# Performance work log

Measured on AMD Instinct MI355X. Metric: run time of the kernel, lower is better.

The kernel has to match this reference:

```python
import jax, jax.numpy as jnp
import numpy as np

N = 20000          # nodes
F = 64             # num_features
H = 128            # hidden_channels
K = 6              # kNN neighbors (includes self, matching torch_cluster.knn(x, x, k))
E = 120000         # unused edge_index length


def knn_indices(x, k):
    # squared euclidean pairwise distances: [N, N]
    sq = jnp.sum(x * x, axis=-1)
    dist2 = sq[:, None] + sq[None, :] - 2.0 * (x @ x.T)
    # k smallest distances per row (self included, dist ~0)
    _, idx = jax.lax.top_k(-dist2, k)   # [N, K]
    return idx


def setup_inputs() -> dict:
    key = jax.random.key(0)
    ks = jax.random.split(key, 6)
    x = jax.random.normal(ks[0], (N, F), dtype=jnp.float32)
    edge_index = jax.random.randint(ks[1], (2, E), 0, N, dtype=jnp.int64)
    W1 = jax.random.normal(ks[2], (2 * F, H), dtype=jnp.float32) * 0.05
    b1 = jnp.zeros((H,), dtype=jnp.float32)
    W2 = jax.random.normal(ks[3], (H, H), dtype=jnp.float32) * 0.05
    b2 = jnp.zeros((H,), dtype=jnp.float32)
    return {"x": x, "edge_index": edge_index, "W1": W1, "b1": b1, "W2": W2, "b2": b2}


def reference(x, edge_index, W1, b1, W2, b2):
    # DynamicEdgeConv: recompute kNN graph each forward (edge_index arg unused, as in source)
    idx = knn_indices(x, K)                       # [N, K] neighbor indices j for each center i
    xi = jnp.broadcast_to(x[:, None, :], (N, K, F))  # center features
    xj = x[idx]                                   # neighbor features  [N, K, F]
    msg = jnp.concatenate([xi, xj - xi], axis=-1)    # [N, K, 2F]
    h = jax.nn.relu(jnp.einsum('nkf,fh->nkh', msg, W1) + b1)
    h = jnp.einsum('nkh,hg->nkg', h, W2) + b2     # [N, K, H]
    return jnp.max(h, axis=1)                     # max aggregation -> [N, H]
```

## Files before the change

kernel.cpp:

```cpp
#include <hip/hip_runtime.h>


#define N_NODES 20000
#define FDIM 64
#define KNN 6
#define HID 128
#define N_PAD 20480
#define NTILES 625
#define PREP_TILES 628
#define NBLK 157
#define NCHUNK 3
#define TPC 209
#define RPB 256
#define TILE_J 64
#define MAX_CHUNKS 10

typedef __attribute__((ext_vector_type(8))) short short8;
typedef __attribute__((ext_vector_type(16))) float f32x16;

#define MFMAB(A, B, C) __builtin_amdgcn_mfma_f32_32x32x16_bf16((A), (B), (C), 0, 0, 0)
#define ROFF(r) (((r) & 3) + 8 * ((r) >> 2))

#define INSERT_CAND(bd, bj, dv, jv) do {                                      \
  if ((dv) < bd[5]) {                                                         \
    const bool c0 = (dv) < bd[0], c1 = (dv) < bd[1], c2 = (dv) < bd[2];       \
    const bool c3 = (dv) < bd[3], c4 = (dv) < bd[4];                          \
    bd[5] = c4 ? bd[4] : (dv);              bj[5] = c4 ? bj[4] : (jv);        \
    bd[4] = c4 ? (c3 ? bd[3] : (dv)) : bd[4]; bj[4] = c4 ? (c3 ? bj[3] : (jv)) : bj[4]; \
    bd[3] = c3 ? (c2 ? bd[2] : (dv)) : bd[3]; bj[3] = c3 ? (c2 ? bj[2] : (jv)) : bj[3]; \
    bd[2] = c2 ? (c1 ? bd[1] : (dv)) : bd[2]; bj[2] = c2 ? (c1 ? bj[1] : (jv)) : bj[2]; \
    bd[1] = c1 ? (c0 ? bd[0] : (dv)) : bd[1]; bj[1] = c1 ? (c0 ? bj[0] : (jv)) : bj[1]; \
    bd[0] = c0 ? (dv) : bd[0];              bj[0] = c0 ? (jv) : bj[0];        \
  }                                                                           \
} while (0)

#define LEXLT(dv, jv, ds, js) (((dv) < (ds)) || ((dv) == (ds) && (jv) < (js)))
#define INSERT_TIE(bd, bj, dv, jv) do {                                       \
  if (LEXLT((dv), (jv), bd[5], bj[5])) {                                      \
    const bool c0 = LEXLT((dv), (jv), bd[0], bj[0]);                          \
    const bool c1 = LEXLT((dv), (jv), bd[1], bj[1]);                          \
    const bool c2 = LEXLT((dv), (jv), bd[2], bj[2]);                          \
    const bool c3 = LEXLT((dv), (jv), bd[3], bj[3]);                          \
    const bool c4 = LEXLT((dv), (jv), bd[4], bj[4]);                          \
    bd[5] = c4 ? bd[4] : (dv);              bj[5] = c4 ? bj[4] : (jv);        \
    bd[4] = c4 ? (c3 ? bd[3] : (dv)) : bd[4]; bj[4] = c4 ? (c3 ? bj[3] : (jv)) : bj[4]; \
    bd[3] = c3 ? (c2 ? bd[2] : (dv)) : bd[3]; bj[3] = c3 ? (c2 ? bj[2] : (jv)) : bj[3]; \
    bd[2] = c2 ? (c1 ? bd[1] : (dv)) : bd[2]; bj[2] = c2 ? (c1 ? bj[1] : (jv)) : bj[2]; \
    bd[1] = c1 ? (c0 ? bd[0] : (dv)) : bd[1]; bj[1] = c1 ? (c0 ? bj[0] : (jv)) : bj[1]; \
    bd[0] = c0 ? (dv) : bd[0];              bj[0] = c0 ? (jv) : bj[0];        \
  }                                                                           \
} while (0)

__device__ __forceinline__ f32x16 zero16() {
  f32x16 v;
#pragma unroll
  for (int i = 0; i < 16; ++i) v[i] = 0.f;
  return v;
}

__device__ __forceinline__ unsigned short bf16_rne(float x) {
  unsigned u = __float_as_uint(x);
  u += 0x7fffu + ((u >> 16) & 1u);
  return (unsigned short)(u >> 16);
}
__device__ __forceinline__ float bf16_tof(unsigned short h) {
  return __uint_as_float(((unsigned)h) << 16);
}

__device__ __forceinline__ void gload_lds16(const void* g, void* l) {
  __builtin_amdgcn_global_load_lds(
      (const __attribute__((address_space(1))) void*)g,
      (__attribute__((address_space(3))) void*)l, 16, 0, 0);
}

__global__ void prep_kernel(const float* __restrict__ x, short* __restrict__ xa,
                            short* __restrict__ xb, short* __restrict__ xc,
                            float* __restrict__ sq) {
  const int n = blockIdx.x * blockDim.x + threadIdx.x;
  if (n >= PREP_TILES * 32) return;
  const int tile = n >> 5, row = n & 31;
  unsigned short a[FDIM], b[FDIM], c[FDIM];
  float s = 0.f;
  if (n < N_NODES) {
    const float4* r4 = (const float4*)(x + (size_t)n * FDIM);
#pragma unroll
    for (int q = 0; q < 16; ++q) {
      const float4 v = r4[q];
      const float vv[4] = {v.x, v.y, v.z, v.w};
#pragma unroll
      for (int e = 0; e < 4; ++e) {
        const float xv = vv[e];
        s = fmaf(xv, xv, s);
        const unsigned short ua = bf16_rne(xv);
        const float r1 = xv - bf16_tof(ua);
        const unsigned short ub = bf16_rne(r1);
        const float r2 = r1 - bf16_tof(ub);
        a[q * 4 + e] = ua; b[q * 4 + e] = ub; c[q * 4 + e] = bf16_rne(r2);
      }
    }
  } else {
#pragma unroll
    for (int f = 0; f < FDIM; ++f) { a[f] = 0; b[f] = 0; c[f] = 0; }
    s = __builtin_inff();
  }
  sq[n] = s;
#pragma unroll
  for (int ks = 0; ks < 4; ++ks) {
#pragma unroll
    for (int hh = 0; hh < 2; ++hh) {
      short8 va, vb, vc;
#pragma unroll
      for (int j = 0; j < 8; ++j) {
        const int f = ks * 16 + hh * 8 + j;
        va[j] = (short)a[f]; vb[j] = (short)b[f]; vc[j] = (short)c[f];
      }
      const size_t off = (size_t)tile * 2048 + ks * 512 + (size_t)((hh << 5) | row) * 8;
      *(short8*)(xa + off) = va;
      *(short8*)(xb + off) = vb;
      *(short8*)(xc + off) = vc;
    }
  }
}

__device__ __forceinline__ void load_frag(const short* __restrict__ xa,
                                          const short* __restrict__ xb,
                                          const short* __restrict__ xc, int t,
                                          int lane, short8 (&Fa)[4],
                                          short8 (&Fb)[4], short8 (&Fc)[4]) {
  const size_t tb = (size_t)t * 2048 + (size_t)lane * 8;
#pragma unroll
  for (int ks = 0; ks < 4; ++ks) {
    Fa[ks] = *(const short8*)(xa + tb + ks * 512);
    Fb[ks] = *(const short8*)(xb + tb + ks * 512);
    Fc[ks] = *(const short8*)(xc + tb + ks * 512);
  }
}

__device__ __forceinline__ void do_select(const f32x16& acc,
                                          const float* __restrict__ sq, int t,
                                          int h, float (&bd)[KNN],
                                          int (&bj)[KNN]) {
  const int sbase = t * 32 + 4 * h;
  float4 S4[4];
#pragma unroll
  for (int g = 0; g < 4; ++g) S4[g] = *(const float4*)(sq + sbase + 8 * g);
  const float sqa[16] = {S4[0].x, S4[0].y, S4[0].z, S4[0].w,
                         S4[1].x, S4[1].y, S4[1].z, S4[1].w,
                         S4[2].x, S4[2].y, S4[2].z, S4[2].w,
                         S4[3].x, S4[3].y, S4[3].z, S4[3].w};
  float key[16];
#pragma unroll
  for (int r = 0; r < 16; ++r) key[r] = fmaf(-2.f, acc[r], sqa[r]);
  float m8[8];
#pragma unroll
  for (int r = 0; r < 8; ++r) m8[r] = fminf(key[r], key[r + 8]);
  float m4[4];
#pragma unroll
  for (int r = 0; r < 4; ++r) m4[r] = fminf(m8[r], m8[r + 4]);
  const float m2a = fminf(m4[0], m4[2]), m2b = fminf(m4[1], m4[3]);
  const float m = fminf(m2a, m2b);
  if (__any(m < bd[5])) {
    const int jbase = t * 32 + 4 * h;
#pragma unroll
    for (int r = 0; r < 16; ++r) { INSERT_CAND(bd, bj, key[r], jbase + ROFF(r)); }
  }
}

__device__ __forceinline__ void xmerge(float (&bd)[KNN], int (&bj)[KNN]) {
  float od[KNN];
  int oj[KNN];
#pragma unroll
  for (int k = 0; k < KNN; ++k) {
    od[k] = __shfl_xor(bd[k], 32);
    oj[k] = __shfl_xor(bj[k], 32);
  }
#pragma unroll
  for (int k = 0; k < KNN; ++k) INSERT_TIE(bd, bj, od[k], oj[k]);
}

__global__ __launch_bounds__(256, 2) void knn_bf16_kernel(
    const short* __restrict__ xa, const short* __restrict__ xb,
    const short* __restrict__ xc, const float* __restrict__ sq,
    float* __restrict__ cand_d, unsigned short* __restrict__ cand_js,
    int* __restrict__ knn_idx, int nchunks) {
  __shared__ __align__(16) short sa[2][2048];
  __shared__ __align__(16) short sb[2][2048];
  __shared__ __align__(16) short sc[2][2048];
  const int tid = threadIdx.x;
  const int lane = tid & 63;
  const int w = tid >> 6;
  const int ct = blockIdx.x * 4 + w;
  const int jc = blockIdx.y;
  const int h = lane >> 5, col = lane & 31;

  short8 Ba[4], Bb[4], Bc[4];
  load_frag(xa, xb, xc, ct, lane, Ba, Bb, Bc);

  float bd[KNN];
  int bj[KNN];
#pragma unroll
  for (int k = 0; k < KNN; ++k) { bd[k] = __builtin_inff(); bj[k] = 0; }

  const int tbeg = jc * TPC;
  int tend = tbeg + TPC;
  if (tend > NTILES) tend = NTILES;
  const int n = tend - tbeg;

  const int wo = w * 512;
  const int go = wo + lane * 8;
  const int la8 = lane * 8;

#define STAGE(set, t)                                                         \
  do {                                                                        \
    const size_t tb_ = (size_t)(t) * 2048 + go;                               \
    gload_lds16(xa + tb_, &sa[set][wo]);                                      \
    gload_lds16(xb + tb_, &sb[set][wo]);                                      \
    gload_lds16(xc + tb_, &sc[set][wo]);                                      \
  } while (0)

#define COMPUTE_TILE(set, accvar)                                             \
  do {                                                                        \
    accvar = zero16();                                                        \
    _Pragma("unroll")                                                         \
    for (int ks = 0; ks < 4; ++ks) {                                          \
      const int o_ = ks * 512 + la8;                                          \
      const short8 Aa = *(const short8*)(&sa[set][o_]);                       \
      const short8 Ab = *(const short8*)(&sb[set][o_]);                       \
      const short8 Ac = *(const short8*)(&sc[set][o_]);                       \
      accvar = MFMAB(Aa, Ba[ks], accvar);                                     \
      accvar = MFMAB(Aa, Bb[ks], accvar);                                     \
      accvar = MFMAB(Ab, Ba[ks], accvar);                                     \
      accvar = MFMAB(Aa, Bc[ks], accvar);                                     \
      accvar = MFMAB(Ac, Ba[ks], accvar);                                     \
      accvar = MFMAB(Ab, Bb[ks], accvar);                                     \
    }                                                                         \
  } while (0)

  STAGE(0, tbeg);
  __syncthreads();
  if (n > 1) STAGE(1, tbeg + 1);
  f32x16 acA, acB;
  COMPUTE_TILE(0, acA);
  __syncthreads();

  int i = 1;
  for (; i + 1 < n; i += 2) {
    STAGE(0, tbeg + i + 1);
    COMPUTE_TILE(1, acB);
    do_select(acA, sq, tbeg + i - 1, h, bd, bj);
    __syncthreads();
    if (i + 2 < n) STAGE(1, tbeg + i + 2);
    COMPUTE_TILE(0, acA);
    do_select(acB, sq, tbeg + i, h, bd, bj);
    __syncthreads();
  }
  if (i < n) {
    COMPUTE_TILE(1, acB);
    do_select(acA, sq, tbeg + i - 1, h, bd, bj);
    do_select(acB, sq, tbeg + i, h, bd, bj);
  } else {
    do_select(acA, sq, tbeg + n - 1, h, bd, bj);
  }
#undef STAGE
#undef COMPUTE_TILE

  xmerge(bd, bj);

  if (h == 0) {
    const int i0 = ct * 32 + col;
    if (i0 < N_NODES) {
      if (nchunks == 1) {
#pragma unroll
        for (int k = 0; k < KNN; ++k) knn_idx[(size_t)i0 * KNN + k] = bj[k];
      } else {
#pragma unroll
        for (int k = 0; k < KNN; ++k) {
          const size_t off = ((size_t)jc * KNN + k) * N_PAD + i0;
          cand_d[off] = bd[k];
          cand_js[off] = (unsigned short)bj[k];
        }
      }
    }
  }
}

__global__ void knn_merge_u16_kernel(const float* __restrict__ cand_d,
                                     const unsigned short* __restrict__ cand_js,
                                     int* __restrict__ knn_idx, int nchunks) {
  const int i = blockIdx.x * blockDim.x + threadIdx.x;
  if (i >= N_NODES) return;
  float bd[KNN];
  int bj[KNN];
#pragma unroll
  for (int k = 0; k < KNN; ++k) { bd[k] = __builtin_inff(); bj[k] = 0; }
  for (int jc = 0; jc < nchunks; ++jc) {
#pragma unroll
    for (int k = 0; k < KNN; ++k) {
      const size_t off = ((size_t)jc * KNN + k) * N_PAD + i;
      const float d = cand_d[off];
      const int j = (int)cand_js[off];
      INSERT_CAND(bd, bj, d, j);
    }
  }
#pragma unroll
  for (int k = 0; k < KNN; ++k) knn_idx[(size_t)i * KNN + k] = bj[k];
}

__global__ void sq_kernel(const float* __restrict__ x, float* __restrict__ sq) {
  const int i = blockIdx.x * blockDim.x + threadIdx.x;
  if (i >= N_NODES) return;
  const float4* r4 = (const float4*)(x + (size_t)i * FDIM);
  float s = 0.f;
#pragma unroll
  for (int q = 0; q < 16; ++q) {
    const float4 a = r4[q];
    s = fmaf(a.x, a.x, s);
    s = fmaf(a.y, a.y, s);
    s = fmaf(a.z, a.z, s);
    s = fmaf(a.w, a.w, s);
  }
  sq[i] = s;
}

__global__ __launch_bounds__(RPB, 2) void knn_partial_kernel(
    const float* __restrict__ x, const float* __restrict__ sq,
    float* __restrict__ cand_d, int* __restrict__ cand_j,
    int* __restrict__ knn_idx, int jchunk, int nchunks) {
  __shared__ __align__(16) float xs[TILE_J][FDIM + 4];
  __shared__ float sqs[TILE_J];
  const int tid = threadIdx.x;
  const int i = blockIdx.x * RPB + tid;
  const bool valid = i < N_NODES;
  const int jc = blockIdx.y;

  float xi[FDIM];
  float sqi = 0.f;
  if (valid) {
    const float4* r4 = (const float4*)(x + (size_t)i * FDIM);
#pragma unroll
    for (int q = 0; q < 16; ++q) {
      const float4 a = r4[q];
      xi[q * 4 + 0] = a.x; xi[q * 4 + 1] = a.y;
      xi[q * 4 + 2] = a.z; xi[q * 4 + 3] = a.w;
    }
    sqi = sq[i];
  } else {
#pragma unroll
    for (int f = 0; f < FDIM; ++f) xi[f] = 0.f;
  }
#pragma unroll
  for (int f = 0; f < FDIM; ++f) asm volatile("" : "+v"(xi[f]));

  float bd[KNN];
  int bj[KNN];
#pragma unroll
  for (int k = 0; k < KNN; ++k) { bd[k] = __builtin_inff(); bj[k] = 0; }

  const int jcbase = jc * jchunk;
  for (int t0 = 0; t0 < jchunk; t0 += TILE_J) {
    const int jt = jcbase + t0;
    __syncthreads();
    {
      const int jj = tid >> 2;
      const int f0 = (tid & 3) * 16;
      const int j = jt + jj;
      float4* dst = (float4*)&xs[jj][f0];
      if (j < N_NODES) {
        const float4* src = (const float4*)(x + (size_t)j * FDIM + f0);
        dst[0] = src[0];
        dst[1] = src[1];
        dst[2] = src[2];
        dst[3] = src[3];
      } else {
        const float4 z = make_float4(0.f, 0.f, 0.f, 0.f);
        dst[0] = z; dst[1] = z; dst[2] = z; dst[3] = z;
      }
      if (tid < TILE_J) {
        const int j2 = jt + tid;
        sqs[tid] = (j2 < N_NODES) ? sq[j2] : 0.f;
      }
    }
    __syncthreads();
    const int rem = N_NODES - jt;
    const int jmax = rem < TILE_J ? rem : TILE_J;
    for (int jj = 0; jj < jmax; ++jj) {
      const float4* xr4 = (const float4*)&xs[jj][0];
      float dot = 0.f;
#pragma unroll
      for (int q = 0; q < 16; ++q) {
        const float4 v = xr4[q];
        dot = fmaf(xi[q * 4 + 0], v.x, dot);
        dot = fmaf(xi[q * 4 + 1], v.y, dot);
        dot = fmaf(xi[q * 4 + 2], v.z, dot);
        dot = fmaf(xi[q * 4 + 3], v.w, dot);
      }
      const float d = fmaf(-2.f, dot, sqi + sqs[jj]);
      const int j = jt + jj;
      INSERT_CAND(bd, bj, d, j);
    }
  }

  if (valid) {
    if (nchunks == 1) {
#pragma unroll
      for (int k = 0; k < KNN; ++k) knn_idx[(size_t)i * KNN + k] = bj[k];
    } else {
#pragma unroll
      for (int k = 0; k < KNN; ++k) {
        const size_t off = ((size_t)jc * KNN + k) * N_PAD + i;
        cand_d[off] = bd[k];
        cand_j[off] = bj[k];
      }
    }
  }
}

__global__ void knn_merge_kernel(const float* __restrict__ cand_d,
                                 const int* __restrict__ cand_j,
                                 int* __restrict__ knn_idx, int nchunks) {
  const int i = blockIdx.x * blockDim.x + threadIdx.x;
  if (i >= N_NODES) return;
  float bd[KNN];
  int bj[KNN];
#pragma unroll
  for (int k = 0; k < KNN; ++k) { bd[k] = __builtin_inff(); bj[k] = 0; }
  for (int jc = 0; jc < nchunks; ++jc) {
#pragma unroll
    for (int k = 0; k < KNN; ++k) {
      const size_t off = ((size_t)jc * KNN + k) * N_PAD + i;
      const float d = cand_d[off];
      const int j = cand_j[off];
      INSERT_CAND(bd, bj, d, j);
    }
  }
#pragma unroll
  for (int k = 0; k < KNN; ++k) knn_idx[(size_t)i * KNN + k] = bj[k];
}

__global__ __launch_bounds__(HID) void mlp_kernel(
    const float* __restrict__ x, const int* __restrict__ knn_idx,
    const float* __restrict__ W1, const float* __restrict__ b1,
    const float* __restrict__ W2, const float* __restrict__ b2,
    float* __restrict__ out) {
  __shared__ float xi_s[FDIM];
  __shared__ float xd_s[KNN][FDIM];
  __shared__ float h1_s[KNN][HID];
  __shared__ int nb[KNN];
  const int i = blockIdx.x;
  const int t = threadIdx.x;
  if (t < KNN) {
    const int v = knn_idx[(size_t)i * KNN + t];
    nb[t] = ((unsigned)v < (unsigned)N_NODES) ? v : 0;
  }
  if (t < FDIM) xi_s[t] = x[(size_t)i * FDIM + t];
  __syncthreads();
  for (int e = t; e < KNN * FDIM; e += HID) {
    const int k = e >> 6;
    const int f = e & 63;
    xd_s[k][f] = x[(size_t)nb[k] * FDIM + f] - xi_s[f];
  }
  __syncthreads();

  float s0 = b1[t];
  for (int f = 0; f < FDIM; ++f) {
    const float w = W1[f * HID + t];
    s0 = fmaf(xi_s[f], w, s0);
  }
  float acc[KNN];
#pragma unroll
  for (int k = 0; k < KNN; ++k) acc[k] = s0;
  for (int f = 0; f < FDIM; ++f) {
    const float w = W1[(FDIM + f) * HID + t];
#pragma unroll
    for (int k = 0; k < KNN; ++k) acc[k] = fmaf(xd_s[k][f], w, acc[k]);
  }
#pragma unroll
  for (int k = 0; k < KNN; ++k) h1_s[k][t] = fmaxf(acc[k], 0.f);
  __syncthreads();

  float acc2[KNN];
  const float bb = b2[t];
#pragma unroll
  for (int k = 0; k < KNN; ++k) acc2[k] = bb;
  for (int h = 0; h < HID; ++h) {
    const float w = W2[h * HID + t];
#pragma unroll
    for (int k = 0; k < KNN; ++k) acc2[k] = fmaf(h1_s[k][h], w, acc2[k]);
  }
  float m = acc2[0];
#pragma unroll
  for (int k = 1; k < KNN; ++k) m = fmaxf(m, acc2[k]);
  out[(size_t)i * HID + t] = m;
}

extern "C" void kernel_launch(void* const* d_in, const int* in_sizes, int n_in,
                              void* d_out, int out_size, void* d_ws, size_t ws_size,
                              hipStream_t stream) {
  const float* x  = (const float*)d_in[0];
  const float* W1 = (const float*)d_in[2];
  const float* b1 = (const float*)d_in[3];
  const float* W2 = (const float*)d_in[4];
  const float* b2 = (const float*)d_in[5];
  float* out = (float*)d_out;
  char* ws = (char*)d_ws;
  const size_t PER_CHUNK = (size_t)KNN * N_PAD * 8;

  if (ws_size >= 0x998000) {
    float* sq   = (float*)ws;
    short* xa   = (short*)(ws + 0x20000);
    short* xb   = (short*)(ws + 0x294000);
    short* xc   = (short*)(ws + 0x508000);
    float* cand_d = (float*)(ws + 0x77C000);
    unsigned short* cand_js = (unsigned short*)(ws + 0x8E4000);
    int* knn = (int*)(ws + 0x20000);

    prep_kernel<<<dim3((PREP_TILES * 32 + 255) / 256), dim3(256), 0, stream>>>(
        x, xa, xb, xc, sq);
    knn_bf16_kernel<<<dim3(NBLK, NCHUNK), dim3(256), 0, stream>>>(
        xa, xb, xc, sq, cand_d, cand_js, knn, NCHUNK);
    knn_merge_u16_kernel<<<dim3((N_NODES + 255) / 256), dim3(256), 0, stream>>>(
        cand_d, cand_js, knn, NCHUNK);
    mlp_kernel<<<dim3(N_NODES), dim3(HID), 0, stream>>>(x, knn, W1, b1, W2, b2, out);
  } else {
    float* sq = (float*)ws;
    int* knn  = (int*)(ws + (size_t)N_PAD * 4);
    const size_t BASE = 0x90000;
    int nc = 1;
    if (ws_size > BASE + PER_CHUNK) {
      size_t fit = (ws_size - BASE) / PER_CHUNK;
      nc = fit < (size_t)MAX_CHUNKS ? (int)fit : MAX_CHUNKS;
      if (nc < 1) nc = 1;
    }
    int jchunk = ((N_NODES + nc - 1) / nc + TILE_J - 1) / TILE_J * TILE_J;
    float* cand_d = (float*)(ws + BASE);
    int* cand_j = (int*)(ws + BASE + (size_t)nc * KNN * N_PAD * 4);

    sq_kernel<<<dim3((N_NODES + 255) / 256), dim3(256), 0, stream>>>(x, sq);
    knn_partial_kernel<<<dim3((N_NODES + RPB - 1) / RPB, nc), dim3(RPB), 0, stream>>>(
        x, sq, cand_d, cand_j, knn, jchunk, nc);
    if (nc > 1) {
      knn_merge_kernel<<<dim3((N_NODES + 255) / 256), dim3(256), 0, stream>>>(
          cand_d, cand_j, knn, nc);
    }
    mlp_kernel<<<dim3(N_NODES), dim3(HID), 0, stream>>>(x, knn, W1, b1, W2, b2, out);
  }
}
```

Baseline: 593.5 us.

## Split each kNN block's column range across two half-workgroups with LDS merge

The kNN kernel now runs 512 threads per block. Two groups of four waves each scan half of the chunk's column tiles, with separate double-buffered LDS tiles per group. The second group's top-k candidates are passed through shared memory and merged by the first group before writing out. This doubles the waves working on each row tile to hide latency and raise occupancy. The cost is more LDS, an extra merge step and barriers, and launch_bounds(512,4) may limit registers and cause spills.

```diff
diff --git a/kernel.cpp b/kernel.cpp
--- a/kernel.cpp
+++ b/kernel.cpp
@@ -178,18 +178,22 @@
   for (int k = 0; k < KNN; ++k) INSERT_TIE(bd, bj, od[k], oj[k]);
 }
 
-__global__ __launch_bounds__(256, 2) void knn_bf16_kernel(
+__global__ __launch_bounds__(512, 4) void knn_bf16_kernel(
     const short* __restrict__ xa, const short* __restrict__ xb,
     const short* __restrict__ xc, const float* __restrict__ sq,
     float* __restrict__ cand_d, unsigned short* __restrict__ cand_js,
     int* __restrict__ knn_idx, int nchunks) {
-  __shared__ __align__(16) short sa[2][2048];
-  __shared__ __align__(16) short sb[2][2048];
-  __shared__ __align__(16) short sc[2][2048];
+  __shared__ __align__(16) short sa[2][2][2048];
+  __shared__ __align__(16) short sb[2][2][2048];
+  __shared__ __align__(16) short sc[2][2][2048];
+  __shared__ float md[4][KNN][32];
+  __shared__ int mj[4][KNN][32];
   const int tid = threadIdx.x;
   const int lane = tid & 63;
   const int w = tid >> 6;
-  const int ct = blockIdx.x * 4 + w;
+  const int wq = w & 3;
+  const int hw = w >> 2;
+  const int ct = blockIdx.x * 4 + wq;
   const int jc = blockIdx.y;
   const int h = lane >> 5, col = lane & 31;
 
@@ -204,18 +208,22 @@
   const int tbeg = jc * TPC;
   int tend = tbeg + TPC;
   if (tend > NTILES) tend = NTILES;
-  const int n = tend - tbeg;
-
-  const int wo = w * 512;
-  const int go = wo + lane * 8;
+  const int span = tend - tbeg;
+  const int len0 = (span + 1) >> 1;
+  const int len1 = span - len0;
+  const int mylen = hw ? len1 : len0;
+  const int rbeg = tbeg + (hw ? len0 : 0);
+  const int N0 = len0;
+
+  const int wo = wq * 512;
   const int la8 = lane * 8;
 
-#define STAGE(set, t)                                                         \
+#define STAGE(set, idx)                                                       \
   do {                                                                        \
-    const size_t tb_ = (size_t)(t) * 2048 + go;                               \
-    gload_lds16(xa + tb_, &sa[set][wo]);                                      \
-    gload_lds16(xb + tb_, &sb[set][wo]);                                      \
-    gload_lds16(xc + tb_, &sc[set][wo]);                                      \
+    const size_t tb_ = (size_t)(rbeg + (idx)) * 2048 + wo + la8;              \
+    gload_lds16(xa + tb_, &sa[set][hw][wo]);                                  \
+    gload_lds16(xb + tb_, &sb[set][hw][wo]);                                  \
+    gload_lds16(xc + tb_, &sc[set][hw][wo]);                                  \
   } while (0)
 
 #define COMPUTE_TILE(set, accvar)                                             \
@@ -224,9 +232,9 @@
     _Pragma("unroll")                                                         \
     for (int ks = 0; ks < 4; ++ks) {                                          \
       const int o_ = ks * 512 + la8;                                          \
-      const short8 Aa = *(const short8*)(&sa[set][o_]);                       \
-      const short8 Ab = *(const short8*)(&sb[set][o_]);                       \
-      const short8 Ac = *(const short8*)(&sc[set][o_]);                       \
+      const short8 Aa = *(const short8*)(&sa[set][hw][o_]);                   \
+      const short8 Ab = *(const short8*)(&sb[set][hw][o_]);                   \
+      const short8 Ac = *(const short8*)(&sc[set][hw][o_]);                   \
       accvar = MFMAB(Aa, Ba[ks], accvar);                                     \
       accvar = MFMAB(Aa, Bb[ks], accvar);                                     \
       accvar = MFMAB(Ab, Ba[ks], accvar);                                     \
@@ -236,37 +244,52 @@
     }                                                                         \
   } while (0)
 
-  STAGE(0, tbeg);
-  __syncthreads();
-  if (n > 1) STAGE(1, tbeg + 1);
+  STAGE(0, 0);
+  __syncthreads();
+  if (1 < mylen) STAGE(1, 1);
   f32x16 acA, acB;
   COMPUTE_TILE(0, acA);
   __syncthreads();
 
   int i = 1;
-  for (; i + 1 < n; i += 2) {
-    STAGE(0, tbeg + i + 1);
-    COMPUTE_TILE(1, acB);
-    do_select(acA, sq, tbeg + i - 1, h, bd, bj);
+  for (; i + 1 < N0; i += 2) {
+    if (i + 1 < mylen) STAGE(0, i + 1);
+    if (i < mylen) COMPUTE_TILE(1, acB);
+    if (i - 1 < mylen) do_select(acA, sq, rbeg + i - 1, h, bd, bj);
     __syncthreads();
-    if (i + 2 < n) STAGE(1, tbeg + i + 2);
-    COMPUTE_TILE(0, acA);
-    do_select(acB, sq, tbeg + i, h, bd, bj);
+    if (i + 2 < mylen) STAGE(1, i + 2);
+    if (i + 1 < mylen) COMPUTE_TILE(0, acA);
+    if (i < mylen) do_select(acB, sq, rbeg + i, h, bd, bj);
     __syncthreads();
   }
-  if (i < n) {
-    COMPUTE_TILE(1, acB);
-    do_select(acA, sq, tbeg + i - 1, h, bd, bj);
-    do_select(acB, sq, tbeg + i, h, bd, bj);
+  if (i < N0) {
+    if (i < mylen) COMPUTE_TILE(1, acB);
+    if (i - 1 < mylen) do_select(acA, sq, rbeg + i - 1, h, bd, bj);
+    if (i < mylen) do_select(acB, sq, rbeg + i, h, bd, bj);
   } else {
-    do_select(acA, sq, tbeg + n - 1, h, bd, bj);
+    if (i - 1 < mylen) do_select(acA, sq, rbeg + i - 1, h, bd, bj);
   }
 #undef STAGE
 #undef COMPUTE_TILE
 
   xmerge(bd, bj);
 
-  if (h == 0) {
+  __syncthreads();
+  if (hw == 1 && h == 0) {
+#pragma unroll
+    for (int k = 0; k < KNN; ++k) {
+      md[wq][k][col] = bd[k];
+      mj[wq][k][col] = bj[k];
+    }
+  }
+  __syncthreads();
+  if (hw == 0 && h == 0) {
+#pragma unroll
+    for (int k = 0; k < KNN; ++k) {
+      const float dv = md[wq][k][col];
+      const int jv = mj[wq][k][col];
+      INSERT_TIE(bd, bj, dv, jv);
+    }
     const int i0 = ct * 32 + col;
     if (i0 < N_NODES) {
       if (nchunks == 1) {
@@ -516,7 +539,7 @@
 
     prep_kernel<<<dim3((PREP_TILES * 32 + 255) / 256), dim3(256), 0, stream>>>(
         x, xa, xb, xc, sq);
-    knn_bf16_kernel<<<dim3(NBLK, NCHUNK), dim3(256), 0, stream>>>(
+    knn_bf16_kernel<<<dim3(NBLK, NCHUNK), dim3(512), 0, stream>>>(
         xa, xb, xc, sq, cand_d, cand_js, knn, NCHUNK);
     knn_merge_u16_kernel<<<dim3((N_NODES + 255) / 256), dim3(256), 0, stream>>>(
         cand_d, cand_js, knn, NCHUNK);
```

Measured after the change: 554.6 us. -6.6%, faster.
